# Kernel tuning notes

Measured on AMD Instinct MI355X. Metric: run time of the kernel, lower is better.

## Reference

```python
import jax, jax.numpy as jnp
import numpy as np

N_ACTOR = 128
NUM_MODS = 6
NUM_PTS = 30
N = 32768
B = 64
EPS = 1e-5


def _gn(x, g, b):
    # torch GroupNorm(1, C) on [..., C]: normalize over channel axis, affine
    m = jnp.mean(x, axis=-1, keepdims=True)
    v = jnp.mean((x - m) ** 2, axis=-1, keepdims=True)
    return (x - m) * jax.lax.rsqrt(v + EPS) * g + b


def setup_inputs() -> dict:
    key = jax.random.key(0)
    ks = jax.random.split(key, 32)
    d = N_ACTOR
    M = NUM_MODS
    s = 0.05
    rn = lambda k, shp: jax.random.normal(k, shp, jnp.float32) * s
    inp = {
        'actors': jax.random.normal(ks[0], (N, d), jnp.float32),
        'actor_ctrs': jax.random.normal(ks[1], (N, 2), jnp.float32),
        'actor_idcs': jnp.arange(N, dtype=jnp.int32).reshape(B, N // B),
        # per-mode residual MLP + output linear (stacked over modes)
        'pred_W1': rn(ks[2], (M, d, d)),
        'pred_g1': jnp.ones((M, d), jnp.float32),
        'pred_b1': jnp.zeros((M, d), jnp.float32),
        'pred_W2': rn(ks[3], (M, d, d)),
        'pred_g2': jnp.ones((M, d), jnp.float32),
        'pred_b2': jnp.zeros((M, d), jnp.float32),
        'pred_Wo': rn(ks[4], (M, d, 2 * NUM_PTS)),
        'pred_bo': rn(ks[5], (M, 2 * NUM_PTS)),
        # cls head: residual MLP + Linear(d,1)
        'cls_W1': rn(ks[6], (d, d)),
        'cls_g1': jnp.ones((d,), jnp.float32),
        'cls_b1': jnp.zeros((d,), jnp.float32),
        'cls_W2': rn(ks[7], (d, d)),
        'cls_g2': jnp.ones((d,), jnp.float32),
        'cls_b2': jnp.zeros((d,), jnp.float32),
        'cls_Wo': rn(ks[8], (d, 1)),
        'cls_bo': rn(ks[9], (1,)),
        # AttDest
        'att_dW1': rn(ks[10], (2, d)),
        'att_db1': rn(ks[11], (d,)),
        'att_dW2': rn(ks[12], (d, d)),
        'att_dg2': jnp.ones((d,), jnp.float32),
        'att_db2': jnp.zeros((d,), jnp.float32),
        'att_aW': rn(ks[13], (2 * d, d)),
        'att_ag': jnp.ones((d,), jnp.float32),
        'att_ab': jnp.zeros((d,), jnp.float32),
    }
    return inp


def reference(actors, actor_ctrs, actor_idcs, pred_W1, pred_g1, pred_b1,
              pred_W2, pred_g2, pred_b2, pred_Wo, pred_bo,
              cls_W1, cls_g1, cls_b1, cls_W2, cls_g2, cls_b2, cls_Wo, cls_bo,
              att_dW1, att_db1, att_dW2, att_dg2, att_db2,
              att_aW, att_ag, att_ab):
    n = actors.shape[0]
    M = pred_W1.shape[0]
    h = jnp.einsum('nc,mcd->mnd', actors, pred_W1)              # [M,N,d]
    h = jax.nn.relu(_gn(h, pred_g1[:, None, :], pred_b1[:, None, :]))
    h = _gn(jnp.einsum('mnd,mde->mne', h, pred_W2),
            pred_g2[:, None, :], pred_b2[:, None, :])
    h = jax.nn.relu(h + actors[None])                           # residual
    preds = jnp.einsum('mnd,mdo->mno', h, pred_Wo) + pred_bo[:, None, :]
    reg = preds.transpose(1, 0, 2).reshape(n, M, NUM_PTS, 2)    # [N,M,T,2]
    # per-scene reg[idcs] += ctrs: actor_idcs partitions arange(N), so this
    # is exactly a per-actor broadcast add of the (concatenated) centers
    reg = reg + actor_ctrs[:, None, None, :]
    dest_ctrs = jax.lax.stop_gradient(reg[:, :, -1, :])         # .detach()
    # --- AttDest ---
    dist = (actor_ctrs[:, None, :] - dest_ctrs).reshape(-1, 2)  # [N*M,2]
    dist = jax.nn.relu(dist @ att_dW1 + att_db1)
    dist = jax.nn.relu(_gn(dist @ att_dW2, att_dg2, att_db2))
    agts = jnp.broadcast_to(actors[:, None, :], (n, M, actors.shape[1]))
    agts = agts.reshape(-1, actors.shape[1])
    feats = jax.nn.relu(_gn(jnp.concatenate([dist, agts], axis=1) @ att_aW,
                            att_ag, att_ab))                    # [N*M,d]
    # --- cls head ---
    c = jax.nn.relu(_gn(feats @ cls_W1, cls_g1, cls_b1))
    c = _gn(c @ cls_W2, cls_g2, cls_b2)
    c = jax.nn.relu(c + feats)
    cls = (c @ cls_Wo + cls_bo).reshape(n, M)
    # --- sort modes by descending score, reorder reg accordingly ---
    order = jnp.argsort(-cls, axis=1)
    cls = jnp.take_along_axis(cls, order, axis=1)
    reg = jnp.take_along_axis(reg, order[:, :, None, None], axis=1)
    # train_model=True concatenates the per-scene splits back in order,
    # which reproduces the full arrays
    return cls, reg
```

## Files before the change

### kernel.cpp

```cpp
#include <hip/hip_runtime.h>

#define EPSV 1e-5f
#define CLS_SZ (32768*6)

#define AL(ch,row) (((ch)<<7) + ((row) ^ ((((ch)&15))<<3)))

__device__ __forceinline__ float4 ld4(const float* p) { return *reinterpret_cast<const float4*>(p); }
__device__ __forceinline__ void st4(float* p, float4 v) { *reinterpret_cast<float4*>(p) = v; }

__device__ __forceinline__ void gemmA(const float* X, const float* __restrict__ Wg,
                                      float* WB0, float* WB1, float (&acc)[8][8],
                                      int ag, int jg4, int tid)
{
  float4 rA = ld4(Wg + tid*4);
  float4 rB = ld4(Wg + 1024 + tid*4);
  __syncthreads();
  st4(WB0 + tid*4, rA);
  st4(WB1 + tid*4, rB);
  __syncthreads();
  #pragma unroll 1
  for (int c = 0; c < 16; ++c) {
    float4 rN;
    const bool pf = (c + 2 < 16);
    if (pf) rN = ld4(Wg + (c+2)*1024 + tid*4);
    const float* WB = (c & 1) ? WB1 : WB0;
    #pragma unroll
    for (int kk = 0; kk < 8; ++kk) {
      int k = c*8 + kk;
      const float* xp = X + (k<<7) + ((ag<<3) ^ ((k & 15)<<3));
      float4 x0 = ld4(xp), x1 = ld4(xp + 4);
      float4 wl = ld4(WB + (kk<<7) + jg4);
      float4 wh = ld4(WB + (kk<<7) + 64 + jg4);
      float xv[8] = {x0.x,x0.y,x0.z,x0.w,x1.x,x1.y,x1.z,x1.w};
      float wv[8] = {wl.x,wl.y,wl.z,wl.w,wh.x,wh.y,wh.z,wh.w};
      #pragma unroll
      for (int r = 0; r < 8; ++r)
        #pragma unroll
        for (int c2 = 0; c2 < 8; ++c2)
          acc[r][c2] = fmaf(xv[r], wv[c2], acc[r][c2]);
    }
    __syncthreads();
    if (pf) st4(((c & 1) ? WB1 : WB0) + tid*4, rN);
  }
}

__device__ __forceinline__ void gemmB(const float* X, const float* __restrict__ Wg,
                                      float* WB0, float* WB1, float (&acc)[4][8],
                                      int ag, int jg4, int tid)
{
  float4 rA, rB;
  const bool wload = tid < 256;
  if (wload) { rA = ld4(Wg + tid*4); rB = ld4(Wg + 1024 + tid*4); }
  __syncthreads();
  if (wload) { st4(WB0 + tid*4, rA); st4(WB1 + tid*4, rB); }
  __syncthreads();
  #pragma unroll 1
  for (int c = 0; c < 16; ++c) {
    float4 rN;
    const bool pf = wload && (c + 2 < 16);
    if (pf) rN = ld4(Wg + (c+2)*1024 + tid*4);
    const float* WB = (c & 1) ? WB1 : WB0;
    #pragma unroll
    for (int kk = 0; kk < 8; ++kk) {
      int k = c*8 + kk;
      float4 x = ld4(X + (k<<7) + ((ag<<2) ^ ((k & 15)<<3)));
      float4 wl = ld4(WB + (kk<<7) + jg4);
      float4 wh = ld4(WB + (kk<<7) + 64 + jg4);
      float xv[4] = {x.x,x.y,x.z,x.w};
      float wv[8] = {wl.x,wl.y,wl.z,wl.w,wh.x,wh.y,wh.z,wh.w};
      #pragma unroll
      for (int r = 0; r < 4; ++r)
        #pragma unroll
        for (int c2 = 0; c2 < 8; ++c2)
          acc[r][c2] = fmaf(xv[r], wv[c2], acc[r][c2]);
    }
    __syncthreads();
    if (pf) st4(((c & 1) ? WB1 : WB0) + tid*4, rN);
  }
}

__device__ __forceinline__ void gemmWo(const float* X, const float* __restrict__ Wg,
                                       float* WB0, float* WB1, float (&acc)[8][4],
                                       int ag, int jg, int tid)
{
  const bool ld = tid < 120;
  const bool zp = (tid >= 120 && tid < 128);
  const int kk0 = ld ? (tid / 15) : (tid - 120);
  const int sl  = ld ? (tid % 15) * 4 : 60;
  float4 rA = {0,0,0,0}, rB = {0,0,0,0};
  if (ld) { rA = ld4(Wg + kk0*60 + sl); rB = ld4(Wg + 480 + kk0*60 + sl); }
  __syncthreads();
  if (ld || zp) { st4(WB0 + (kk0<<6) + sl, rA); st4(WB1 + (kk0<<6) + sl, rB); }
  __syncthreads();
  #pragma unroll 1
  for (int c = 0; c < 16; ++c) {
    float4 rN = {0,0,0,0};
    const bool pf = (c + 2 < 16);
    if (pf && ld) rN = ld4(Wg + (c+2)*480 + kk0*60 + sl);
    const float* WB = (c & 1) ? WB1 : WB0;
    #pragma unroll
    for (int kk = 0; kk < 8; ++kk) {
      int k = c*8 + kk;
      const float* xp = X + (k<<7) + ((ag<<3) ^ ((k & 15)<<3));
      float4 x0 = ld4(xp), x1 = ld4(xp + 4);
      float4 w = ld4(WB + (kk<<6) + jg*4);
      float xv[8] = {x0.x,x0.y,x0.z,x0.w,x1.x,x1.y,x1.z,x1.w};
      float wv[4] = {w.x,w.y,w.z,w.w};
      #pragma unroll
      for (int r = 0; r < 8; ++r)
        #pragma unroll
        for (int c2 = 0; c2 < 4; ++c2)
          acc[r][c2] = fmaf(xv[r], wv[c2], acc[r][c2]);
    }
    __syncthreads();
    if (pf && (ld || zp)) st4(((c & 1) ? WB1 : WB0) + (kk0<<6) + sl, rN);
  }
}

__device__ __forceinline__ void gn_finish(float* PS1, float* PS2, float* MEAN, float* RSTD, int tid)
{
  __syncthreads();
  if (tid < 128) {
    float a = 0.f, b = 0.f;
    #pragma unroll
    for (int j = 0; j < 4; ++j) { a += PS1[tid*5 + j]; b += PS2[tid*5 + j]; }
    float mu = a * 0.0078125f;
    float var = b * 0.0078125f - mu*mu;
    MEAN[tid] = mu;
    RSTD[tid] = rsqrtf(var + EPSV);
  }
  __syncthreads();
}

__device__ __forceinline__ void gn_reduce8(const float (&acc)[8][8], float* PS1, float* PS2,
                                           float* MEAN, float* RSTD, int ag, int jg, int tid)
{
  #pragma unroll
  for (int r = 0; r < 8; ++r) {
    float s = 0.f, q = 0.f;
    #pragma unroll
    for (int c = 0; c < 8; ++c) { float v = acc[r][c]; s += v; q += v*v; }
    s += __shfl_xor(s, 1, 64); q += __shfl_xor(q, 1, 64);
    s += __shfl_xor(s, 2, 64); q += __shfl_xor(q, 2, 64);
    if ((jg & 3) == 0) { int row = ag*8 + r; PS1[row*5 + (jg>>2)] = s; PS2[row*5 + (jg>>2)] = q; }
  }
  gn_finish(PS1, PS2, MEAN, RSTD, tid);
}

__device__ __forceinline__ void gn_reduce4(const float (&acc)[4][8], float* PS1, float* PS2,
                                           float* MEAN, float* RSTD, int ag, int jg, int tid)
{
  #pragma unroll
  for (int r = 0; r < 4; ++r) {
    float s = 0.f, q = 0.f;
    #pragma unroll
    for (int c = 0; c < 8; ++c) { float v = acc[r][c]; s += v; q += v*v; }
    s += __shfl_xor(s, 1, 64); q += __shfl_xor(q, 1, 64);
    s += __shfl_xor(s, 2, 64); q += __shfl_xor(q, 2, 64);
    if ((jg & 3) == 0) { int row = ag*4 + r; PS1[row*5 + (jg>>2)] = s; PS2[row*5 + (jg>>2)] = q; }
  }
  gn_finish(PS1, PS2, MEAN, RSTD, tid);
}

__global__ void __launch_bounds__(256, 2) pred_kernel(
    const float* __restrict__ actors, const float* __restrict__ ctrs,
    const float* __restrict__ W1, const float* __restrict__ g1v, const float* __restrict__ b1v,
    const float* __restrict__ W2, const float* __restrict__ g2v, const float* __restrict__ b2v,
    const float* __restrict__ Wo, const float* __restrict__ bov,
    float* __restrict__ out_reg)
{
  __shared__ __align__(16) float ACT[16384];
  __shared__ __align__(16) float WB0[1024], WB1[1024];
  __shared__ float PS1[640], PS2[640], MEAN[128], RSTD[128];

  const int tid = threadIdx.x;
  const int jg = tid & 15, ag = tid >> 4;
  const int jg4 = jg*4;
  const int m  = blockIdx.y;
  const int n0 = blockIdx.x * 128;

  #pragma unroll
  for (int p = 0; p < 16; ++p) {
    int i = (p<<8) + tid;
    int r = i >> 5, q4 = (i & 31) << 2;
    float4 v = ld4(actors + (size_t)(n0 + r)*128 + q4);
    ACT[AL(q4+0, r)] = v.x; ACT[AL(q4+1, r)] = v.y;
    ACT[AL(q4+2, r)] = v.z; ACT[AL(q4+3, r)] = v.w;
  }

  float acc[8][8];
  #pragma unroll
  for (int r = 0; r < 8; ++r)
    #pragma unroll
    for (int c = 0; c < 8; ++c) acc[r][c] = 0.f;

  gemmA(ACT, W1 + (size_t)m*16384, WB0, WB1, acc, ag, jg4, tid);
  gn_reduce8(acc, PS1, PS2, MEAN, RSTD, ag, jg, tid);
  {
    float mu[8], rs[8];
    #pragma unroll
    for (int r = 0; r < 8; ++r) { mu[r] = MEAN[ag*8+r]; rs[r] = RSTD[ag*8+r]; }
    float4 gl = ld4(g1v + m*128 + jg4), gh = ld4(g1v + m*128 + 64 + jg4);
    float4 bl = ld4(b1v + m*128 + jg4), bh = ld4(b1v + m*128 + 64 + jg4);
    float gv[8] = {gl.x,gl.y,gl.z,gl.w,gh.x,gh.y,gh.z,gh.w};
    float bv[8] = {bl.x,bl.y,bl.z,bl.w,bh.x,bh.y,bh.z,bh.w};
    float vm[8][8];
    #pragma unroll
    for (int r = 0; r < 8; ++r)
      #pragma unroll
      for (int c = 0; c < 8; ++c)
        vm[r][c] = fmaxf((acc[r][c] - mu[r]) * rs[r] * gv[c] + bv[c], 0.f);
    #pragma unroll
    for (int c = 0; c < 8; ++c) {
      int ch = (c < 4) ? (jg4 + c) : (64 + jg4 + (c - 4));
      int base = (ch<<7) + ((ag<<3) ^ ((ch & 15)<<3));
      st4(ACT + base,     make_float4(vm[0][c],vm[1][c],vm[2][c],vm[3][c]));
      st4(ACT + base + 4, make_float4(vm[4][c],vm[5][c],vm[6][c],vm[7][c]));
    }
  }

  #pragma unroll
  for (int r = 0; r < 8; ++r)
    #pragma unroll
    for (int c = 0; c < 8; ++c) acc[r][c] = 0.f;

  gemmA(ACT, W2 + (size_t)m*16384, WB0, WB1, acc, ag, jg4, tid);
  gn_reduce8(acc, PS1, PS2, MEAN, RSTD, ag, jg, tid);
  {
    float mu[8], rs[8];
    #pragma unroll
    for (int r = 0; r < 8; ++r) { mu[r] = MEAN[ag*8+r]; rs[r] = RSTD[ag*8+r]; }
    float4 gl = ld4(g2v + m*128 + jg4), gh = ld4(g2v + m*128 + 64 + jg4);
    float4 bl = ld4(b2v + m*128 + jg4), bh = ld4(b2v + m*128 + 64 + jg4);
    float gv[8] = {gl.x,gl.y,gl.z,gl.w,gh.x,gh.y,gh.z,gh.w};
    float bv[8] = {bl.x,bl.y,bl.z,bl.w,bh.x,bh.y,bh.z,bh.w};
    float vm[8][8];
    #pragma unroll
    for (int r = 0; r < 8; ++r) {
      const float* ap = actors + (size_t)(n0 + ag*8 + r)*128;
      float4 a0 = ld4(ap + jg4), a1 = ld4(ap + 64 + jg4);
      float av[8] = {a0.x,a0.y,a0.z,a0.w,a1.x,a1.y,a1.z,a1.w};
      #pragma unroll
      for (int c = 0; c < 8; ++c)
        vm[r][c] = fmaxf((acc[r][c] - mu[r]) * rs[r] * gv[c] + bv[c] + av[c], 0.f);
    }
    #pragma unroll
    for (int c = 0; c < 8; ++c) {
      int ch = (c < 4) ? (jg4 + c) : (64 + jg4 + (c - 4));
      int base = (ch<<7) + ((ag<<3) ^ ((ch & 15)<<3));
      st4(ACT + base,     make_float4(vm[0][c],vm[1][c],vm[2][c],vm[3][c]));
      st4(ACT + base + 4, make_float4(vm[4][c],vm[5][c],vm[6][c],vm[7][c]));
    }
  }

  float acc2[8][4];
  #pragma unroll
  for (int r = 0; r < 8; ++r)
    #pragma unroll
    for (int c = 0; c < 4; ++c) acc2[r][c] = 0.f;
  gemmWo(ACT, Wo + (size_t)m*7680, WB0, WB1, acc2, ag, jg, tid);

  if (jg < 15) {
    float4 bo4 = ld4(bov + m*60 + jg4);
    #pragma unroll
    for (int r = 0; r < 8; ++r) {
      int n = n0 + ag*8 + r;
      float2 cc = *reinterpret_cast<const float2*>(ctrs + 2*n);
      float4 v;
      v.x = acc2[r][0] + bo4.x + cc.x;
      v.y = acc2[r][1] + bo4.y + cc.y;
      v.z = acc2[r][2] + bo4.z + cc.x;
      v.w = acc2[r][3] + bo4.w + cc.y;
      st4(out_reg + (size_t)n*360 + m*60 + jg4, v);
    }
  }
}

__global__ void __launch_bounds__(512, 2) att_cls_kernel(
    const float* __restrict__ actors, const float* __restrict__ ctrs,
    const float* __restrict__ dW1, const float* __restrict__ db1,
    const float* __restrict__ dW2, const float* __restrict__ dg2, const float* __restrict__ db2,
    const float* __restrict__ aW, const float* __restrict__ aG, const float* __restrict__ aB,
    const float* __restrict__ cW1, const float* __restrict__ cg1, const float* __restrict__ cb1,
    const float* __restrict__ cW2, const float* __restrict__ cg2, const float* __restrict__ cb2,
    const float* __restrict__ cWo, const float* __restrict__ cbo,
    const float* __restrict__ reg, float* __restrict__ cls_out)
{
  __shared__ __align__(16) float ACT[16384];
  __shared__ __align__(16) float WB0[1024], WB1[1024];
  __shared__ float PS1[640], PS2[640], MEAN[128], RSTD[128], D0x[128], D0y[128];

  const int tid = threadIdx.x;
  const int jg = tid & 15, ag = tid >> 4;
  const int jg4 = jg*4;
  const int r0 = blockIdx.x * 128;

  if (tid < 128) {
    int rg = r0 + tid;
    int n = rg / 6, mm = rg - 6*n;
    size_t base = (size_t)n*360 + mm*60;
    float2 c2 = *reinterpret_cast<const float2*>(ctrs + 2*n);
    D0x[tid] = c2.x - reg[base + 58];
    D0y[tid] = c2.y - reg[base + 59];
  }
  __syncthreads();

  {
    float dx[4], dy[4];
    #pragma unroll
    for (int r = 0; r < 4; ++r) { dx[r] = D0x[ag*4+r]; dy[r] = D0y[ag*4+r]; }
    #pragma unroll
    for (int c = 0; c < 8; ++c) {
      int ch = (c < 4) ? (jg4 + c) : (64 + jg4 + (c - 4));
      float w1 = dW1[ch], w2 = dW1[128 + ch], bb = db1[ch];
      float4 v;
      v.x = fmaxf(fmaf(dx[0], w1, fmaf(dy[0], w2, bb)), 0.f);
      v.y = fmaxf(fmaf(dx[1], w1, fmaf(dy[1], w2, bb)), 0.f);
      v.z = fmaxf(fmaf(dx[2], w1, fmaf(dy[2], w2, bb)), 0.f);
      v.w = fmaxf(fmaf(dx[3], w1, fmaf(dy[3], w2, bb)), 0.f);
      st4(ACT + (ch<<7) + ((ag<<2) ^ ((ch & 15)<<3)), v);
    }
  }

  float acc[4][8];
  #pragma unroll
  for (int r = 0; r < 4; ++r)
    #pragma unroll
    for (int c = 0; c < 8; ++c) acc[r][c] = 0.f;

  gemmB(ACT, dW2, WB0, WB1, acc, ag, jg4, tid);
  gn_reduce4(acc, PS1, PS2, MEAN, RSTD, ag, jg, tid);
  {
    float mu[4], rs[4];
    #pragma unroll
    for (int r = 0; r < 4; ++r) { mu[r] = MEAN[ag*4+r]; rs[r] = RSTD[ag*4+r]; }
    float4 gl = ld4(dg2 + jg4), gh = ld4(dg2 + 64 + jg4);
    float4 bl = ld4(db2 + jg4), bh = ld4(db2 + 64 + jg4);
    float gv[8] = {gl.x,gl.y,gl.z,gl.w,gh.x,gh.y,gh.z,gh.w};
    float bv[8] = {bl.x,bl.y,bl.z,bl.w,bh.x,bh.y,bh.z,bh.w};
    #pragma unroll
    for (int c = 0; c < 8; ++c) {
      int ch = (c < 4) ? (jg4 + c) : (64 + jg4 + (c - 4));
      float4 v;
      v.x = fmaxf((acc[0][c] - mu[0]) * rs[0] * gv[c] + bv[c], 0.f);
      v.y = fmaxf((acc[1][c] - mu[1]) * rs[1] * gv[c] + bv[c], 0.f);
      v.z = fmaxf((acc[2][c] - mu[2]) * rs[2] * gv[c] + bv[c], 0.f);
      v.w = fmaxf((acc[3][c] - mu[3]) * rs[3] * gv[c] + bv[c], 0.f);
      st4(ACT + (ch<<7) + ((ag<<2) ^ ((ch & 15)<<3)), v);
    }
  }

  #pragma unroll
  for (int r = 0; r < 4; ++r)
    #pragma unroll
    for (int c = 0; c < 8; ++c) acc[r][c] = 0.f;
  gemmB(ACT, aW, WB0, WB1, acc, ag, jg4, tid);
  #pragma unroll
  for (int p = 0; p < 8; ++p) {
    int i = (p<<9) + tid;
    int r = i >> 5, q4 = (i & 31) << 2;
    int n = (r0 + r) / 6;
    float4 v = ld4(actors + (size_t)n*128 + q4);
    ACT[AL(q4+0, r)] = v.x; ACT[AL(q4+1, r)] = v.y;
    ACT[AL(q4+2, r)] = v.z; ACT[AL(q4+3, r)] = v.w;
  }
  gemmB(ACT, aW + 16384, WB0, WB1, acc, ag, jg4, tid);
  gn_reduce4(acc, PS1, PS2, MEAN, RSTD, ag, jg, tid);
  float feats[4][8];
  {
    float mu[4], rs[4];
    #pragma unroll
    for (int r = 0; r < 4; ++r) { mu[r] = MEAN[ag*4+r]; rs[r] = RSTD[ag*4+r]; }
    float4 gl = ld4(aG + jg4), gh = ld4(aG + 64 + jg4);
    float4 bl = ld4(aB + jg4), bh = ld4(aB + 64 + jg4);
    float gv[8] = {gl.x,gl.y,gl.z,gl.w,gh.x,gh.y,gh.z,gh.w};
    float bv[8] = {bl.x,bl.y,bl.z,bl.w,bh.x,bh.y,bh.z,bh.w};
    #pragma unroll
    for (int r = 0; r < 4; ++r)
      #pragma unroll
      for (int c = 0; c < 8; ++c)
        feats[r][c] = fmaxf((acc[r][c] - mu[r]) * rs[r] * gv[c] + bv[c], 0.f);
    #pragma unroll
    for (int c = 0; c < 8; ++c) {
      int ch = (c < 4) ? (jg4 + c) : (64 + jg4 + (c - 4));
      st4(ACT + (ch<<7) + ((ag<<2) ^ ((ch & 15)<<3)),
          make_float4(feats[0][c],feats[1][c],feats[2][c],feats[3][c]));
    }
  }

  #pragma unroll
  for (int r = 0; r < 4; ++r)
    #pragma unroll
    for (int c = 0; c < 8; ++c) acc[r][c] = 0.f;
  gemmB(ACT, cW1, WB0, WB1, acc, ag, jg4, tid);
  gn_reduce4(acc, PS1, PS2, MEAN, RSTD, ag, jg, tid);
  {
    float mu[4], rs[4];
    #pragma unroll
    for (int r = 0; r < 4; ++r) { mu[r] = MEAN[ag*4+r]; rs[r] = RSTD[ag*4+r]; }
    float4 gl = ld4(cg1 + jg4), gh = ld4(cg1 + 64 + jg4);
    float4 bl = ld4(cb1 + jg4), bh = ld4(cb1 + 64 + jg4);
    float gv[8] = {gl.x,gl.y,gl.z,gl.w,gh.x,gh.y,gh.z,gh.w};
    float bv[8] = {bl.x,bl.y,bl.z,bl.w,bh.x,bh.y,bh.z,bh.w};
    #pragma unroll
    for (int c = 0; c < 8; ++c) {
      int ch = (c < 4) ? (jg4 + c) : (64 + jg4 + (c - 4));
      float4 v;
      v.x = fmaxf((acc[0][c] - mu[0]) * rs[0] * gv[c] + bv[c], 0.f);
      v.y = fmaxf((acc[1][c] - mu[1]) * rs[1] * gv[c] + bv[c], 0.f);
      v.z = fmaxf((acc[2][c] - mu[2]) * rs[2] * gv[c] + bv[c], 0.f);
      v.w = fmaxf((acc[3][c] - mu[3]) * rs[3] * gv[c] + bv[c], 0.f);
      st4(ACT + (ch<<7) + ((ag<<2) ^ ((ch & 15)<<3)), v);
    }
  }

  #pragma unroll
  for (int r = 0; r < 4; ++r)
    #pragma unroll
    for (int c = 0; c < 8; ++c) acc[r][c] = 0.f;
  gemmB(ACT, cW2, WB0, WB1, acc, ag, jg4, tid);
  gn_reduce4(acc, PS1, PS2, MEAN, RSTD, ag, jg, tid);
  {
    float mu[4], rs[4], p[4] = {0.f, 0.f, 0.f, 0.f};
    #pragma unroll
    for (int r = 0; r < 4; ++r) { mu[r] = MEAN[ag*4+r]; rs[r] = RSTD[ag*4+r]; }
    float4 gl = ld4(cg2 + jg4), gh = ld4(cg2 + 64 + jg4);
    float4 bl = ld4(cb2 + jg4), bh = ld4(cb2 + 64 + jg4);
    float4 wl = ld4(cWo + jg4), wh = ld4(cWo + 64 + jg4);
    float gv[8] = {gl.x,gl.y,gl.z,gl.w,gh.x,gh.y,gh.z,gh.w};
    float bv[8] = {bl.x,bl.y,bl.z,bl.w,bh.x,bh.y,bh.z,bh.w};
    float wv[8] = {wl.x,wl.y,wl.z,wl.w,wh.x,wh.y,wh.z,wh.w};
    #pragma unroll
    for (int c = 0; c < 8; ++c) {
      p[0] = fmaf(fmaxf((acc[0][c] - mu[0]) * rs[0] * gv[c] + bv[c] + feats[0][c], 0.f), wv[c], p[0]);
      p[1] = fmaf(fmaxf((acc[1][c] - mu[1]) * rs[1] * gv[c] + bv[c] + feats[1][c], 0.f), wv[c], p[1]);
      p[2] = fmaf(fmaxf((acc[2][c] - mu[2]) * rs[2] * gv[c] + bv[c] + feats[2][c], 0.f), wv[c], p[2]);
      p[3] = fmaf(fmaxf((acc[3][c] - mu[3]) * rs[3] * gv[c] + bv[c] + feats[3][c], 0.f), wv[c], p[3]);
    }
    #pragma unroll
    for (int r = 0; r < 4; ++r) {
      float s = p[r];
      s += __shfl_xor(s, 1, 64);
      s += __shfl_xor(s, 2, 64);
      if ((jg & 3) == 0) PS1[(ag*4+r)*5 + (jg>>2)] = s;
    }
  }
  __syncthreads();
  if (tid < 128) {
    float s = 0.f;
    #pragma unroll
    for (int j = 0; j < 4; ++j) s += PS1[tid*5 + j];
    cls_out[r0 + tid] = s + cbo[0];
  }
}

__global__ void __launch_bounds__(256) sort_kernel(float* __restrict__ out)
{
  __shared__ float RL[64*360];
  __shared__ float CL[64*6];
  __shared__ float CS[64*6];
  __shared__ int   ORD[64*6];

  const int tid = threadIdx.x;
  const int n0 = blockIdx.x * 64;
  float* regp = out + CLS_SZ;

  for (int i = tid; i < 64*360; i += 256) RL[i] = regp[(size_t)n0*360 + i];
  for (int i = tid; i < 384; i += 256)    CL[i] = out[n0*6 + i];
  __syncthreads();

  if (tid < 64) {
    float v[6];
    #pragma unroll
    for (int m2 = 0; m2 < 6; ++m2) v[m2] = CL[tid*6 + m2];
    int used = 0;
    for (int j = 0; j < 6; ++j) {
      int best = -1; float bv = 0.f;
      for (int m2 = 0; m2 < 6; ++m2) {
        if (used & (1 << m2)) continue;
        if (best < 0 || v[m2] > bv) { best = m2; bv = v[m2]; }
      }
      used |= (1 << best);
      ORD[tid*6 + j] = best;
      CS[tid*6 + j] = bv;
    }
  }
  __syncthreads();

  for (int i = tid; i < 384; i += 256) out[n0*6 + i] = CS[i];
  for (int i = tid; i < 64*360; i += 256) {
    int rl = i / 360, rem = i - rl*360;
    int slot = rem / 60, j = rem - slot*60;
    out[CLS_SZ + (size_t)n0*360 + i] = RL[rl*360 + ORD[rl*6 + slot]*60 + j];
  }
}

extern "C" void kernel_launch(void* const* d_in, const int* in_sizes, int n_in,
                              void* d_out, int out_size, void* d_ws, size_t ws_size,
                              hipStream_t stream)
{
  (void)in_sizes; (void)n_in; (void)out_size; (void)d_ws; (void)ws_size;
  const float* actors = (const float*)d_in[0];
  const float* ctrs   = (const float*)d_in[1];
  const float* pW1 = (const float*)d_in[3];
  const float* pg1 = (const float*)d_in[4];
  const float* pb1 = (const float*)d_in[5];
  const float* pW2 = (const float*)d_in[6];
  const float* pg2 = (const float*)d_in[7];
  const float* pb2 = (const float*)d_in[8];
  const float* pWo = (const float*)d_in[9];
  const float* pbo = (const float*)d_in[10];
  const float* cW1 = (const float*)d_in[11];
  const float* cg1 = (const float*)d_in[12];
  const float* cb1 = (const float*)d_in[13];
  const float* cW2 = (const float*)d_in[14];
  const float* cg2 = (const float*)d_in[15];
  const float* cb2 = (const float*)d_in[16];
  const float* cWo = (const float*)d_in[17];
  const float* cbo = (const float*)d_in[18];
  const float* dW1 = (const float*)d_in[19];
  const float* db1 = (const float*)d_in[20];
  const float* dW2 = (const float*)d_in[21];
  const float* dg2 = (const float*)d_in[22];
  const float* db2 = (const float*)d_in[23];
  const float* aW  = (const float*)d_in[24];
  const float* aG  = (const float*)d_in[25];
  const float* aB  = (const float*)d_in[26];

  float* out = (float*)d_out;
  float* out_reg = out + CLS_SZ;

  dim3 gA(256, 6);
  pred_kernel<<<gA, 256, 0, stream>>>(actors, ctrs, pW1, pg1, pb1, pW2, pg2, pb2,
                                      pWo, pbo, out_reg);
  att_cls_kernel<<<1536, 512, 0, stream>>>(actors, ctrs,
                                           dW1, db1, dW2, dg2, db2,
                                           aW, aG, aB,
                                           cW1, cg1, cb1, cW2, cg2, cb2, cWo, cbo,
                                           out_reg, out);
  sort_kernel<<<512, 256, 0, stream>>>(out);
}
```

Before: 856.7 us.

## Use 256-thread blocks with 8x8 register tiles in att_cls kernel; alias reduction scratch

The attention/cls kernel goes from 512 threads holding 4x8 accumulator tiles to 256 threads holding 8x8 tiles, reusing the gemmA path already used by the pred kernel. Each thread now does more FMAs per shared-memory load, which cuts LDS traffic per flop. The GroupNorm partial-sum buffers and the distance scratch now alias the weight double-buffers and the MEAN/RSTD arrays, shrinking static shared memory. In exchange, register pressure per thread rises and there are fewer threads per block to hide latency.

```diff
diff --git a/kernel.cpp b/kernel.cpp
--- a/kernel.cpp
+++ b/kernel.cpp
@@ -44,41 +44,6 @@
   }
 }
 
-__device__ __forceinline__ void gemmB(const float* X, const float* __restrict__ Wg,
-                                      float* WB0, float* WB1, float (&acc)[4][8],
-                                      int ag, int jg4, int tid)
-{
-  float4 rA, rB;
-  const bool wload = tid < 256;
-  if (wload) { rA = ld4(Wg + tid*4); rB = ld4(Wg + 1024 + tid*4); }
-  __syncthreads();
-  if (wload) { st4(WB0 + tid*4, rA); st4(WB1 + tid*4, rB); }
-  __syncthreads();
-  #pragma unroll 1
-  for (int c = 0; c < 16; ++c) {
-    float4 rN;
-    const bool pf = wload && (c + 2 < 16);
-    if (pf) rN = ld4(Wg + (c+2)*1024 + tid*4);
-    const float* WB = (c & 1) ? WB1 : WB0;
-    #pragma unroll
-    for (int kk = 0; kk < 8; ++kk) {
-      int k = c*8 + kk;
-      float4 x = ld4(X + (k<<7) + ((ag<<2) ^ ((k & 15)<<3)));
-      float4 wl = ld4(WB + (kk<<7) + jg4);
-      float4 wh = ld4(WB + (kk<<7) + 64 + jg4);
-      float xv[4] = {x.x,x.y,x.z,x.w};
-      float wv[8] = {wl.x,wl.y,wl.z,wl.w,wh.x,wh.y,wh.z,wh.w};
-      #pragma unroll
-      for (int r = 0; r < 4; ++r)
-        #pragma unroll
-        for (int c2 = 0; c2 < 8; ++c2)
-          acc[r][c2] = fmaf(xv[r], wv[c2], acc[r][c2]);
-    }
-    __syncthreads();
-    if (pf) st4(((c & 1) ? WB1 : WB0) + tid*4, rN);
-  }
-}
-
 __device__ __forceinline__ void gemmWo(const float* X, const float* __restrict__ Wg,
                                        float* WB0, float* WB1, float (&acc)[8][4],
                                        int ag, int jg, int tid)
@@ -123,7 +88,7 @@
   if (tid < 128) {
     float a = 0.f, b = 0.f;
     #pragma unroll
-    for (int j = 0; j < 4; ++j) { a += PS1[tid*5 + j]; b += PS2[tid*5 + j]; }
+    for (int j = 0; j < 4; ++j) { a += PS1[tid*4 + j]; b += PS2[tid*4 + j]; }
     float mu = a * 0.0078125f;
     float var = b * 0.0078125f - mu*mu;
     MEAN[tid] = mu;
@@ -142,22 +107,7 @@
     for (int c = 0; c < 8; ++c) { float v = acc[r][c]; s += v; q += v*v; }
     s += __shfl_xor(s, 1, 64); q += __shfl_xor(q, 1, 64);
     s += __shfl_xor(s, 2, 64); q += __shfl_xor(q, 2, 64);
-    if ((jg & 3) == 0) { int row = ag*8 + r; PS1[row*5 + (jg>>2)] = s; PS2[row*5 + (jg>>2)] = q; }
-  }
-  gn_finish(PS1, PS2, MEAN, RSTD, tid);
-}
-
-__device__ __forceinline__ void gn_reduce4(const float (&acc)[4][8], float* PS1, float* PS2,
-                                           float* MEAN, float* RSTD, int ag, int jg, int tid)
-{
-  #pragma unroll
-  for (int r = 0; r < 4; ++r) {
-    float s = 0.f, q = 0.f;
-    #pragma unroll
-    for (int c = 0; c < 8; ++c) { float v = acc[r][c]; s += v; q += v*v; }
-    s += __shfl_xor(s, 1, 64); q += __shfl_xor(q, 1, 64);
-    s += __shfl_xor(s, 2, 64); q += __shfl_xor(q, 2, 64);
-    if ((jg & 3) == 0) { int row = ag*4 + r; PS1[row*5 + (jg>>2)] = s; PS2[row*5 + (jg>>2)] = q; }
+    if ((jg & 3) == 0) { int row = ag*8 + r; PS1[row*4 + (jg>>2)] = s; PS2[row*4 + (jg>>2)] = q; }
   }
   gn_finish(PS1, PS2, MEAN, RSTD, tid);
 }
@@ -171,7 +121,9 @@
 {
   __shared__ __align__(16) float ACT[16384];
   __shared__ __align__(16) float WB0[1024], WB1[1024];
-  __shared__ float PS1[640], PS2[640], MEAN[128], RSTD[128];
+  __shared__ float MEAN[128], RSTD[128];
+  float* PS1 = WB0;
+  float* PS2 = WB1;
 
   const int tid = threadIdx.x;
   const int jg = tid & 15, ag = tid >> 4;
@@ -276,7 +228,7 @@
   }
 }
 
-__global__ void __launch_bounds__(512, 2) att_cls_kernel(
+__global__ void __launch_bounds__(256, 2) att_cls_kernel(
     const float* __restrict__ actors, const float* __restrict__ ctrs,
     const float* __restrict__ dW1, const float* __restrict__ db1,
     const float* __restrict__ dW2, const float* __restrict__ dg2, const float* __restrict__ db2,
@@ -288,7 +240,11 @@
 {
   __shared__ __align__(16) float ACT[16384];
   __shared__ __align__(16) float WB0[1024], WB1[1024];
-  __shared__ float PS1[640], PS2[640], MEAN[128], RSTD[128], D0x[128], D0y[128];
+  __shared__ float MEAN[128], RSTD[128];
+  float* PS1 = WB0;
+  float* PS2 = WB1;
+  float* D0x = MEAN;
+  float* D0y = RSTD;
 
   const int tid = threadIdx.x;
   const int jg = tid & 15, ag = tid >> 4;
@@ -306,124 +262,131 @@
   __syncthreads();
 
   {
-    float dx[4], dy[4];
-    #pragma unroll
-    for (int r = 0; r < 4; ++r) { dx[r] = D0x[ag*4+r]; dy[r] = D0y[ag*4+r]; }
+    float dx[8], dy[8];
+    #pragma unroll
+    for (int r = 0; r < 8; ++r) { dx[r] = D0x[ag*8+r]; dy[r] = D0y[ag*8+r]; }
     #pragma unroll
     for (int c = 0; c < 8; ++c) {
       int ch = (c < 4) ? (jg4 + c) : (64 + jg4 + (c - 4));
       float w1 = dW1[ch], w2 = dW1[128 + ch], bb = db1[ch];
-      float4 v;
-      v.x = fmaxf(fmaf(dx[0], w1, fmaf(dy[0], w2, bb)), 0.f);
-      v.y = fmaxf(fmaf(dx[1], w1, fmaf(dy[1], w2, bb)), 0.f);
-      v.z = fmaxf(fmaf(dx[2], w1, fmaf(dy[2], w2, bb)), 0.f);
-      v.w = fmaxf(fmaf(dx[3], w1, fmaf(dy[3], w2, bb)), 0.f);
-      st4(ACT + (ch<<7) + ((ag<<2) ^ ((ch & 15)<<3)), v);
-    }
-  }
-
-  float acc[4][8];
-  #pragma unroll
-  for (int r = 0; r < 4; ++r)
+      float v[8];
+      #pragma unroll
+      for (int r = 0; r < 8; ++r) v[r] = fmaxf(fmaf(dx[r], w1, fmaf(dy[r], w2, bb)), 0.f);
+      int base = (ch<<7) + ((ag<<3) ^ ((ch & 15)<<3));
+      st4(ACT + base,     make_float4(v[0],v[1],v[2],v[3]));
+      st4(ACT + base + 4, make_float4(v[4],v[5],v[6],v[7]));
+    }
+  }
+
+  float acc[8][8];
+  #pragma unroll
+  for (int r = 0; r < 8; ++r)
     #pragma unroll
     for (int c = 0; c < 8; ++c) acc[r][c] = 0.f;
 
-  gemmB(ACT, dW2, WB0, WB1, acc, ag, jg4, tid);
-  gn_reduce4(acc, PS1, PS2, MEAN, RSTD, ag, jg, tid);
-  {
-    float mu[4], rs[4];
-    #pragma unroll
-    for (int r = 0; r < 4; ++r) { mu[r] = MEAN[ag*4+r]; rs[r] = RSTD[ag*4+r]; }
+  gemmA(ACT, dW2, WB0, WB1, acc, ag, jg4, tid);
+  gn_reduce8(acc, PS1, PS2, MEAN, RSTD, ag, jg, tid);
+  {
+    float mu[8], rs[8];
+    #pragma unroll
+    for (int r = 0; r < 8; ++r) { mu[r] = MEAN[ag*8+r]; rs[r] = RSTD[ag*8+r]; }
     float4 gl = ld4(dg2 + jg4), gh = ld4(dg2 + 64 + jg4);
     float4 bl = ld4(db2 + jg4), bh = ld4(db2 + 64 + jg4);
     float gv[8] = {gl.x,gl.y,gl.z,gl.w,gh.x,gh.y,gh.z,gh.w};
     float bv[8] = {bl.x,bl.y,bl.z,bl.w,bh.x,bh.y,bh.z,bh.w};
+    float vm[8][8];
+    #pragma unroll
+    for (int r = 0; r < 8; ++r)
+      #pragma unroll
+      for (int c = 0; c < 8; ++c)
+        vm[r][c] = fmaxf((acc[r][c] - mu[r]) * rs[r] * gv[c] + bv[c], 0.f);
     #pragma unroll
     for (int c = 0; c < 8; ++c) {
       int ch = (c < 4) ? (jg4 + c) : (64 + jg4 + (c - 4));
-      float4 v;
-      v.x = fmaxf((acc[0][c] - mu[0]) * rs[0] * gv[c] + bv[c], 0.f);
-      v.y = fmaxf((acc[1][c] - mu[1]) * rs[1] * gv[c] + bv[c], 0.f);
-      v.z = fmaxf((acc[2][c] - mu[2]) * rs[2] * gv[c] + bv[c], 0.f);
-      v.w = fmaxf((acc[3][c] - mu[3]) * rs[3] * gv[c] + bv[c], 0.f);
-      st4(ACT + (ch<<7) + ((ag<<2) ^ ((ch & 15)<<3)), v);
-    }
-  }
-
-  #pragma unroll
-  for (int r = 0; r < 4; ++r)
+      int base = (ch<<7) + ((ag<<3) ^ ((ch & 15)<<3));
+      st4(ACT + base,     make_float4(vm[0][c],vm[1][c],vm[2][c],vm[3][c]));
+      st4(ACT + base + 4, make_float4(vm[4][c],vm[5][c],vm[6][c],vm[7][c]));
+    }
+  }
+
+  #pragma unroll
+  for (int r = 0; r < 8; ++r)
     #pragma unroll
     for (int c = 0; c < 8; ++c) acc[r][c] = 0.f;
-  gemmB(ACT, aW, WB0, WB1, acc, ag, jg4, tid);
-  #pragma unroll
-  for (int p = 0; p < 8; ++p) {
-    int i = (p<<9) + tid;
+  gemmA(ACT, aW, WB0, WB1, acc, ag, jg4, tid);
+  #pragma unroll
+  for (int p = 0; p < 16; ++p) {
+    int i = (p<<8) + tid;
     int r = i >> 5, q4 = (i & 31) << 2;
     int n = (r0 + r) / 6;
     float4 v = ld4(actors + (size_t)n*128 + q4);
     ACT[AL(q4+0, r)] = v.x; ACT[AL(q4+1, r)] = v.y;
     ACT[AL(q4+2, r)] = v.z; ACT[AL(q4+3, r)] = v.w;
   }
-  gemmB(ACT, aW + 16384, WB0, WB1, acc, ag, jg4, tid);
-  gn_reduce4(acc, PS1, PS2, MEAN, RSTD, ag, jg, tid);
-  float feats[4][8];
-  {
-    float mu[4], rs[4];
-    #pragma unroll
-    for (int r = 0; r < 4; ++r) { mu[r] = MEAN[ag*4+r]; rs[r] = RSTD[ag*4+r]; }
+  gemmA(ACT, aW + 16384, WB0, WB1, acc, ag, jg4, tid);
+  gn_reduce8(acc, PS1, PS2, MEAN, RSTD, ag, jg, tid);
+  float feats[8][8];
+  {
+    float mu[8], rs[8];
+    #pragma unroll
+    for (int r = 0; r < 8; ++r) { mu[r] = MEAN[ag*8+r]; rs[r] = RSTD[ag*8+r]; }
     float4 gl = ld4(aG + jg4), gh = ld4(aG + 64 + jg4);
     float4 bl = ld4(aB + jg4), bh = ld4(aB + 64 + jg4);
     float gv[8] = {gl.x,gl.y,gl.z,gl.w,gh.x,gh.y,gh.z,gh.w};
     float bv[8] = {bl.x,bl.y,bl.z,bl.w,bh.x,bh.y,bh.z,bh.w};
     #pragma unroll
-    for (int r = 0; r < 4; ++r)
+    for (int r = 0; r < 8; ++r)
       #pragma unroll
       for (int c = 0; c < 8; ++c)
         feats[r][c] = fmaxf((acc[r][c] - mu[r]) * rs[r] * gv[c] + bv[c], 0.f);
     #pragma unroll
     for (int c = 0; c < 8; ++c) {
       int ch = (c < 4) ? (jg4 + c) : (64 + jg4 + (c - 4));
-      st4(ACT + (ch<<7) + ((ag<<2) ^ ((ch & 15)<<3)),
-          make_float4(feats[0][c],feats[1][c],feats[2][c],feats[3][c]));
-    }
-  }
-
-  #pragma unroll
-  for (int r = 0; r < 4; ++r)
+      int base = (ch<<7) + ((ag<<3) ^ ((ch & 15)<<3));
+      st4(ACT + base,     make_float4(feats[0][c],feats[1][c],feats[2][c],feats[3][c]));
+      st4(ACT + base + 4, make_float4(feats[4][c],feats[5][c],feats[6][c],feats[7][c]));
+    }
+  }
+
+  #pragma unroll
+  for (int r = 0; r < 8; ++r)
     #pragma unroll
     for (int c = 0; c < 8; ++c) acc[r][c] = 0.f;
-  gemmB(ACT, cW1, WB0, WB1, acc, ag, jg4, tid);
-  gn_reduce4(acc, PS1, PS2, MEAN, RSTD, ag, jg, tid);
-  {
-    float mu[4], rs[4];
-    #pragma unroll
-    for (int r = 0; r < 4; ++r) { mu[r] = MEAN[ag*4+r]; rs[r] = RSTD[ag*4+r]; }
+  gemmA(ACT, cW1, WB0, WB1, acc, ag, jg4, tid);
+  gn_reduce8(acc, PS1, PS2, MEAN, RSTD, ag, jg, tid);
+  {
+    float mu[8], rs[8];
+    #pragma unroll
+    for (int r = 0; r < 8; ++r) { mu[r] = MEAN[ag*8+r]; rs[r] = RSTD[ag*8+r]; }
     float4 gl = ld4(cg1 + jg4), gh = ld4(cg1 + 64 + jg4);
     float4 bl = ld4(cb1 + jg4), bh = ld4(cb1 + 64 + jg4);
     float gv[8] = {gl.x,gl.y,gl.z,gl.w,gh.x,gh.y,gh.z,gh.w};
     float bv[8] = {bl.x,bl.y,bl.z,bl.w,bh.x,bh.y,bh.z,bh.w};
+    float vm[8][8];
+    #pragma unroll
+    for (int r = 0; r < 8; ++r)
+      #pragma unroll
+      for (int c = 0; c < 8; ++c)
+        vm[r][c] = fmaxf((acc[r][c] - mu[r]) * rs[r] * gv[c] + bv[c], 0.f);
     #pragma unroll
     for (int c = 0; c < 8; ++c) {
       int ch = (c < 4) ? (jg4 + c) : (64 + jg4 + (c - 4));
-      float4 v;
-      v.x = fmaxf((acc[0][c] - mu[0]) * rs[0] * gv[c] + bv[c], 0.f);
-      v.y = fmaxf((acc[1][c] - mu[1]) * rs[1] * gv[c] + bv[c], 0.f);
-      v.z = fmaxf((acc[2][c] - mu[2]) * rs[2] * gv[c] + bv[c], 0.f);
-      v.w = fmaxf((acc[3][c] - mu[3]) * rs[3] * gv[c] + bv[c], 0.f);
-      st4(ACT + (ch<<7) + ((ag<<2) ^ ((ch & 15)<<3)), v);
-    }
-  }
-
-  #pragma unroll
-  for (int r = 0; r < 4; ++r)
+      int base = (ch<<7) + ((ag<<3) ^ ((ch & 15)<<3));
+      st4(ACT + base,     make_float4(vm[0][c],vm[1][c],vm[2][c],vm[3][c]));
+      st4(ACT + base + 4, make_float4(vm[4][c],vm[5][c],vm[6][c],vm[7][c]));
+    }
+  }
+
+  #pragma unroll
+  for (int r = 0; r < 8; ++r)
     #pragma unroll
     for (int c = 0; c < 8; ++c) acc[r][c] = 0.f;
-  gemmB(ACT, cW2, WB0, WB1, acc, ag, jg4, tid);
-  gn_reduce4(acc, PS1, PS2, MEAN, RSTD, ag, jg, tid);
-  {
-    float mu[4], rs[4], p[4] = {0.f, 0.f, 0.f, 0.f};
-    #pragma unroll
-    for (int r = 0; r < 4; ++r) { mu[r] = MEAN[ag*4+r]; rs[r] = RSTD[ag*4+r]; }
+  gemmA(ACT, cW2, WB0, WB1, acc, ag, jg4, tid);
+  gn_reduce8(acc, PS1, PS2, MEAN, RSTD, ag, jg, tid);
+  {
+    float mu[8], rs[8], p[8];
+    #pragma unroll
+    for (int r = 0; r < 8; ++r) { mu[r] = MEAN[ag*8+r]; rs[r] = RSTD[ag*8+r]; p[r] = 0.f; }
     float4 gl = ld4(cg2 + jg4), gh = ld4(cg2 + 64 + jg4);
     float4 bl = ld4(cb2 + jg4), bh = ld4(cb2 + 64 + jg4);
     float4 wl = ld4(cWo + jg4), wh = ld4(cWo + 64 + jg4);
@@ -432,24 +395,26 @@
     float wv[8] = {wl.x,wl.y,wl.z,wl.w,wh.x,wh.y,wh.z,wh.w};
     #pragma unroll
     for (int c = 0; c < 8; ++c) {
-      p[0] = fmaf(fmaxf((acc[0][c] - mu[0]) * rs[0] * gv[c] + bv[c] + feats[0][c], 0.f), wv[c], p[0]);
-      p[1] = fmaf(fmaxf((acc[1][c] - mu[1]) * rs[1] * gv[c] + bv[c] + feats[1][c], 0.f), wv[c], p[1]);
-      p[2] = fmaf(fmaxf((acc[2][c] - mu[2]) * rs[2] * gv[c] + bv[c] + feats[2][c], 0.f), wv[c], p[2]);
-      p[3] = fmaf(fmaxf((acc[3][c] - mu[3]) * rs[3] * gv[c] + bv[c] + feats[3][c], 0.f), wv[c], p[3]);
-    }
-    #pragma unroll
-    for (int r = 0; r < 4; ++r) {
+      #pragma unroll
+      for (int r = 0; r < 8; ++r) {
+        float v = (acc[r][c] - mu[r]) * rs[r] * gv[c] + bv[c];
+        v = fmaxf(v + feats[r][c], 0.f);
+        p[r] = fmaf(v, wv[c], p[r]);
+      }
+    }
+    #pragma unroll
+    for (int r = 0; r < 8; ++r) {
       float s = p[r];
       s += __shfl_xor(s, 1, 64);
       s += __shfl_xor(s, 2, 64);
-      if ((jg & 3) == 0) PS1[(ag*4+r)*5 + (jg>>2)] = s;
+      if ((jg & 3) == 0) PS1[(ag*8+r)*4 + (jg>>2)] = s;
     }
   }
   __syncthreads();
   if (tid < 128) {
     float s = 0.f;
     #pragma unroll
-    for (int j = 0; j < 4; ++j) s += PS1[tid*5 + j];
+    for (int j = 0; j < 4; ++j) s += PS1[tid*4 + j];
     cls_out[r0 + tid] = s + cbo[0];
   }
 }
@@ -533,7 +498,7 @@
   dim3 gA(256, 6);
   pred_kernel<<<gA, 256, 0, stream>>>(actors, ctrs, pW1, pg1, pb1, pW2, pg2, pb2,
                                       pWo, pbo, out_reg);
-  att_cls_kernel<<<1536, 512, 0, stream>>>(actors, ctrs,
+  att_cls_kernel<<<1536, 256, 0, stream>>>(actors, ctrs,
                                            dW1, db1, dW2, dg2, db2,
                                            aW, aG, aB,
                                            cW1, cg1, cb1, cW2, cg2, cb2, cWo, cbo,
```

New measurement: 753.0 us. 1.14x faster.
